# Kernel tuning notes

Measured on AMD Instinct MI355X. Metric: run time of the kernel, lower is better.

The kernel has to match this reference:

```python
import jax, jax.numpy as jnp
import numpy as np

DT = 0.001
TAU_M = 0.02
TAU_S = 0.005
ALPHA = 1.0 - DT / TAU_S  # synaptic decay = 0.8
BETA = 1.0 - DT / TAU_M   # membrane decay = 0.95


def setup_inputs() -> dict:
    key = jax.random.key(0)
    k1, k2 = jax.random.split(key)
    steps, batch, d1, d2 = 100, 256, 784, 512
    x = (jax.random.uniform(k1, (steps, batch, d1)) < 0.05).astype(jnp.float32)
    # kaiming_normal_ on (d2, d1): std = sqrt(2 / fan_in)
    weight = jax.random.normal(k2, (d2, d1), dtype=jnp.float32) * np.float32(np.sqrt(2.0 / d1))
    return {"x": x, "weight": weight}


def reference(x, weight):
    # x: [steps, batch, d1] spikes; weight: [d2, d1]
    batch = x.shape[1]
    d2 = weight.shape[0]
    zeros = jnp.zeros((batch, d2), dtype=x.dtype)

    def step(carry, x_t):
        I_prev, V_prev = carry
        I = ALPHA * I_prev + x_t @ weight.T            # synaptic current
        V_pre = BETA * V_prev + (1.0 - BETA) * I        # membrane before reset
        s = (V_pre > 1.0).astype(x.dtype)               # threshold crossing
        V = (1.0 - s) * V_pre                           # reset to zero on spike
        return (I, V), s

    # torch loop runs i = 1..steps-1 using input[i-1]; output[0] stays zero
    _, spikes = jax.lax.scan(step, (zeros, zeros), x[:-1])
    return jnp.concatenate([zeros[None], spikes], axis=0)  # [steps, batch, d2]
```

## Files before the change

kernel.cpp:

```cpp
#include <hip/hip_runtime.h>

#define STEPS 100
#define BATCH 256
#define D1 784
#define D1P 785
#define D2 512
#define NSTEP 99
#define NTB (NSTEP * BATCH)
#define LIST_PAD 80
#define ROWB 48

#define L1_LISTS_OFF 0
#define L1_LISTS_BYTES ((size_t)NTB * LIST_PAD * 2)
#define L1_CNTS_OFF  L1_LISTS_BYTES
#define L1_CNTS_BYTES ((size_t)NTB * 4)
#define L1_Z_OFF     (((L1_CNTS_OFF + L1_CNTS_BYTES) + 255) & ~(size_t)255)
#define Z_BYTES      ((size_t)NTB * D2 * 4)
#define WS_T1        (L1_Z_OFF + Z_BYTES)

#define WT_BYTES  (D1P * D2 * 4)
#define T2_Z_OFF  ((size_t)((WT_BYTES + 255) & ~255))
#define WS_T2     (T2_Z_OFF + Z_BYTES)

#define HALF1 392
#define HCAP  64


__global__ __launch_bounds__(256) void prep_lists(
    const float* __restrict__ x, unsigned short* __restrict__ lists,
    unsigned int* __restrict__ cnt8s)
{
    const int wid  = blockIdx.x * 4 + (threadIdx.x >> 6);
    const int lane = threadIdx.x & 63;
    const float* xt = x + (size_t)wid * D1;
    unsigned short* lp = lists + (size_t)wid * LIST_PAD;

    int cnt = 0;
    for (int base = 0; base < D1; base += 64) {
        int i = base + lane;
        bool a = (i < D1) && (xt[i] > 0.5f);
        unsigned long long m = __ballot(a);
        int pre = __popcll(m & ((1ull << lane) - 1ull));
        if (a) {
            int p = cnt + pre;
            if (p < LIST_PAD) lp[p] = (unsigned short)(i * ROWB);
        }
        cnt += __popcll(m);
    }
    if (cnt > LIST_PAD) cnt = LIST_PAD;
    int cnt8 = (cnt + 7) & ~7;
    if (cnt8 < 8) cnt8 = 8;
    if (lane < cnt8 - cnt) lp[cnt + lane] = (unsigned short)(D1 * ROWB);
    if (lane == 0) cnt8s[wid] = (unsigned int)cnt8;
}

__global__ __launch_bounds__(512, 8) void gather_lds(
    const float* __restrict__ W,
    const unsigned short* __restrict__ lists,
    const unsigned int* __restrict__ cnt8s,
    float* __restrict__ z)
{
    const int slice = blockIdx.x & 63;
    const int chunk = blockIdx.x >> 6;
    const int j0 = slice * 8;

    __shared__ __align__(16) float wt[D1P * (ROWB / 4)];

    for (int v = threadIdx.x; v < 8 * D1; v += 512) {
        int jj = v & 7;
        int i  = v >> 3;
        wt[i * (ROWB / 4) + jj] = W[(size_t)(j0 + jj) * D1 + i];
    }
    if (threadIdx.x < (ROWB / 4)) wt[D1 * (ROWB / 4) + threadIdx.x] = 0.f;
    __syncthreads();

    const int tbsub = threadIdx.x >> 1;
    const unsigned int jb = (unsigned int)((threadIdx.x & 1) << 4);
    const char* base = (const char*)wt;
    const int tb0 = chunk * (NTB / 16);
    const int tb1 = tb0 + (NTB / 16);

    for (int tb = tb0 + tbsub; tb < tb1; tb += 256) {
        const unsigned short* lp = lists + (size_t)tb * LIST_PAD;
        const int c8 = (int)cnt8s[tb];
        uint4 r = *(const uint4*)lp;
        float ax = 0.f, ay = 0.f, az = 0.f, aw = 0.f;
        float bx = 0.f, by = 0.f, bz = 0.f, bw = 0.f;
        for (int k = 0; k < c8; k += 8) {
            int kn = k + 8;
            if (kn > c8 - 8) kn = c8 - 8;
            uint4 rn = *(const uint4*)(lp + kn);
            float4 w0 = *(const float4*)(base + ((r.x & 0xFFFFu) + jb));
            float4 w1 = *(const float4*)(base + ((r.x >> 16)     + jb));
            float4 w2 = *(const float4*)(base + ((r.y & 0xFFFFu) + jb));
            float4 w3 = *(const float4*)(base + ((r.y >> 16)     + jb));
            float4 w4 = *(const float4*)(base + ((r.z & 0xFFFFu) + jb));
            float4 w5 = *(const float4*)(base + ((r.z >> 16)     + jb));
            float4 w6 = *(const float4*)(base + ((r.w & 0xFFFFu) + jb));
            float4 w7 = *(const float4*)(base + ((r.w >> 16)     + jb));
            ax += w0.x; ay += w0.y; az += w0.z; aw += w0.w;
            bx += w1.x; by += w1.y; bz += w1.z; bw += w1.w;
            ax += w2.x; ay += w2.y; az += w2.z; aw += w2.w;
            bx += w3.x; by += w3.y; bz += w3.z; bw += w3.w;
            ax += w4.x; ay += w4.y; az += w4.z; aw += w4.w;
            bx += w5.x; by += w5.y; bz += w5.z; bw += w5.w;
            ax += w6.x; ay += w6.y; az += w6.z; aw += w6.w;
            bx += w7.x; by += w7.y; bz += w7.z; bw += w7.w;
            r = rn;
        }
        float4 r4;
        r4.x = ax + bx; r4.y = ay + by; r4.z = az + bz; r4.w = aw + bw;
        *(float4*)(z + (size_t)tb * D2 + j0 + ((threadIdx.x & 1) << 2)) = r4;
    }
}

__global__ __launch_bounds__(256) void lif_scan(
    const float* __restrict__ z, float* __restrict__ out)
{
    const int gid = blockIdx.x * 256 + threadIdx.x;
    out[gid] = 0.f;
    float I = 0.f, V = 0.f;
    const float* zp = z + gid;
    float* op = out + (size_t)(BATCH * D2) + gid;
    for (int t0 = 0; t0 < NSTEP; t0 += 8) {
        const int n = (NSTEP - t0 < 8) ? (NSTEP - t0) : 8;
        float zz[8];
        #pragma unroll
        for (int u = 0; u < 8; ++u)
            if (u < n) zz[u] = zp[(size_t)(t0 + u) * (BATCH * D2)];
        #pragma unroll
        for (int u = 0; u < 8; ++u)
            if (u < n) {
                I = 0.8f * I + zz[u];
                float Vp = 0.95f * V + 0.05f * I;
                float s = (Vp > 1.0f) ? 1.0f : 0.f;
                V = (1.0f - s) * Vp;
                op[(size_t)(t0 + u) * (BATCH * D2)] = s;
            }
    }
}

__global__ void transpose_w(const float* __restrict__ W, float* __restrict__ Wt) {
    __shared__ float tile[32][33];
    int i0 = blockIdx.x * 32;
    int j0 = blockIdx.y * 32;
    int tx = threadIdx.x, ty = threadIdx.y;
    for (int r = 0; r < 32; r += 8) {
        int jj = j0 + ty + r, ii = i0 + tx;
        float v = 0.f;
        if (jj < D2 && ii < D1) v = W[jj * D1 + ii];
        tile[ty + r][tx] = v;
    }
    __syncthreads();
    for (int r = 0; r < 32; r += 8) {
        int ii = i0 + ty + r, jj = j0 + tx;
        if (ii < D1P && jj < D2) Wt[ii * D2 + jj] = tile[tx][ty + r];
    }
}

__global__ __launch_bounds__(512) void gather_z(
    const float* __restrict__ x, const float* __restrict__ Wt,
    float* __restrict__ z)
{
    const int g    = threadIdx.x >> 7;
    const int t128 = threadIdx.x & 127;
    const int half = (threadIdx.x >> 6) & 1;
    const int lane = threadIdx.x & 63;
    const int tb   = blockIdx.x * 4 + g;
    __shared__ __align__(16) unsigned int s_off[4][2][HCAP];
    __shared__ int s_cnt[4][2];
    {
        const float* xh = x + (size_t)tb * D1 + half * HALF1;
        unsigned int* lp = s_off[g][half];
        int cnt = 0;
        for (int base = 0; base < HALF1; base += 64) {
            int i = base + lane;
            bool a = (i < HALF1) && (xh[i] > 0.5f);
            unsigned long long m = __ballot(a);
            int pre = __popcll(m & ((1ull << lane) - 1ull));
            if (a) {
                int p = cnt + pre;
                if (p < HCAP) lp[p] = (unsigned int)((half * HALF1 + i) << 11);
            }
            cnt += __popcll(m);
        }
        if (cnt > HCAP) cnt = HCAP;
        int cnt4 = (cnt + 3) & ~3;
        if (lane < cnt4 - cnt) lp[cnt + lane] = (unsigned int)(D1 << 11);
        if (lane == 0) s_cnt[g][half] = cnt4;
    }
    __syncthreads();
    const char* wj = (const char*)Wt + (t128 << 4);
    float ax0 = 0.f, ay0 = 0.f, az0 = 0.f, aw0 = 0.f;
    float ax1 = 0.f, ay1 = 0.f, az1 = 0.f, aw1 = 0.f;
    #pragma unroll
    for (int h = 0; h < 2; ++h) {
        const unsigned int* l = s_off[g][h];
        const int c4 = s_cnt[g][h];
        for (int k = 0; k < c4; k += 4) {
            uint4 o = *(const uint4*)(l + k);
            float4 w0 = *(const float4*)(wj + o.x);
            float4 w1 = *(const float4*)(wj + o.y);
            float4 w2 = *(const float4*)(wj + o.z);
            float4 w3 = *(const float4*)(wj + o.w);
            ax0 += w0.x; ay0 += w0.y; az0 += w0.z; aw0 += w0.w;
            ax1 += w1.x; ay1 += w1.y; az1 += w1.z; aw1 += w1.w;
            ax0 += w2.x; ay0 += w2.y; az0 += w2.z; aw0 += w2.w;
            ax1 += w3.x; ay1 += w3.y; az1 += w3.z; aw1 += w3.w;
        }
    }
    float4 r;
    r.x = ax0 + ax1; r.y = ay0 + ay1; r.z = az0 + az1; r.w = aw0 + aw1;
    *(float4*)(z + (size_t)tb * D2 + (t128 << 2)) = r;
}

__global__ __launch_bounds__(256) void snn_fallback(
    const float* __restrict__ x, const float* __restrict__ Wfull,
    float* __restrict__ out)
{
    const int b = blockIdx.x >> 1;
    const int jhalf = blockIdx.x & 1;
    const int j = jhalf * 256 + threadIdx.x;
    const int lane = threadIdx.x & 63;
    __shared__ int s_cnt;
    __shared__ int s_list[D1];
    out[(size_t)b * D2 + j] = 0.f;
    float I = 0.f, V = 0.f;
    const float* wrow = Wfull + (size_t)j * D1;
    for (int t = 0; t < STEPS - 1; ++t) {
        if (threadIdx.x == 0) s_cnt = 0;
        __syncthreads();
        const float* xt = x + (size_t)(t * BATCH + b) * D1;
        for (int base = 0; base < D1; base += 256) {
            int i = base + threadIdx.x;
            bool active = (i < D1) && (xt[i] > 0.5f);
            unsigned long long mask = __ballot(active);
            int nact = __popcll(mask);
            int pre = __popcll(mask & ((1ull << lane) - 1ull));
            int wb = 0;
            if (lane == 0 && nact) wb = atomicAdd(&s_cnt, nact);
            wb = __shfl(wb, 0);
            if (active) s_list[wb + pre] = i;
        }
        __syncthreads();
        const int cnt = s_cnt;
        float a0 = 0.f, a1 = 0.f, a2 = 0.f, a3 = 0.f;
        int k = 0;
        for (; k + 4 <= cnt; k += 4) {
            a0 += wrow[s_list[k]];     a1 += wrow[s_list[k + 1]];
            a2 += wrow[s_list[k + 2]]; a3 += wrow[s_list[k + 3]];
        }
        for (; k < cnt; ++k) a0 += wrow[s_list[k]];
        float acc = (a0 + a1) + (a2 + a3);
        I = 0.8f * I + acc;
        float Vp = 0.95f * V + 0.05f * I;
        float s = (Vp > 1.0f) ? 1.0f : 0.f;
        V = (1.0f - s) * Vp;
        out[(size_t)(t + 1) * (BATCH * D2) + (size_t)b * D2 + j] = s;
        __syncthreads();
    }
}

extern "C" void kernel_launch(void* const* d_in, const int* in_sizes, int n_in,
                              void* d_out, int out_size, void* d_ws, size_t ws_size,
                              hipStream_t stream) {
    const float* x = (const float*)d_in[0];
    const float* w = (const float*)d_in[1];
    float* out = (float*)d_out;
    char* ws = (char*)d_ws;

    if (ws_size >= WS_T1) {
        unsigned short* lists = (unsigned short*)(ws + L1_LISTS_OFF);
        unsigned int* cnt8s = (unsigned int*)(ws + L1_CNTS_OFF);
        float* z = (float*)(ws + L1_Z_OFF);
        prep_lists<<<NTB / 4, 256, 0, stream>>>(x, lists, cnt8s);
        gather_lds<<<1024, 512, 0, stream>>>(w, lists, cnt8s, z);
        lif_scan<<<BATCH * D2 / 256, 256, 0, stream>>>(z, out);
    } else if (ws_size >= WS_T2) {
        float* wt = (float*)ws;
        float* z  = (float*)(ws + T2_Z_OFF);
        dim3 tg(25, 16), tb(32, 8);
        transpose_w<<<tg, tb, 0, stream>>>(w, wt);
        gather_z<<<NTB / 4, 512, 0, stream>>>(x, wt, z);
        lif_scan<<<BATCH * D2 / 256, 256, 0, stream>>>(z, out);
    } else {
        snn_fallback<<<BATCH * 2, 256, 0, stream>>>(x, w, out);
    }
}
```

Baseline: 224.3 us.

## Widen gather column slice to 32 outputs per block with eight lanes per row

Each gather block now stages a 32-column slice of the transposed weight in about 100 KB of dynamic LDS instead of an 8-column slice. Eight lanes share each (t,b) spike list and each reads a float4 from one LDS row, so list reads and index decoding are spread over 32 outputs rather than 8. Fewer blocks (256) are launched, and the LIF scan is unrolled 16 steps instead of 8 to keep more loads in flight. In exchange, the large LDS footprint limits occupancy to about one block per CU, and 256 blocks may underfill the GPU.

```diff
diff --git a/kernel.cpp b/kernel.cpp
--- a/kernel.cpp
+++ b/kernel.cpp
@@ -8,7 +8,12 @@
 #define NSTEP 99
 #define NTB (NSTEP * BATCH)
 #define LIST_PAD 80
-#define ROWB 48
+
+#define JS 32
+#define ROWB 128
+#define G32_LDS (D1P * JS * 4)
+#define NCHUNK 16
+#define CHUNK_TB (NTB / NCHUNK)
 
 #define L1_LISTS_OFF 0
 #define L1_LISTS_BYTES ((size_t)NTB * LIST_PAD * 2)
@@ -43,44 +48,56 @@
         int pre = __popcll(m & ((1ull << lane) - 1ull));
         if (a) {
             int p = cnt + pre;
-            if (p < LIST_PAD) lp[p] = (unsigned short)(i * ROWB);
+            if (p < LIST_PAD) lp[p] = (unsigned short)(i << 3);
         }
         cnt += __popcll(m);
     }
     if (cnt > LIST_PAD) cnt = LIST_PAD;
     int cnt8 = (cnt + 7) & ~7;
     if (cnt8 < 8) cnt8 = 8;
-    if (lane < cnt8 - cnt) lp[cnt + lane] = (unsigned short)(D1 * ROWB);
+    if (lane < cnt8 - cnt) lp[cnt + lane] = (unsigned short)(D1 << 3);
     if (lane == 0) cnt8s[wid] = (unsigned int)cnt8;
 }
 
-__global__ __launch_bounds__(512, 8) void gather_lds(
+__global__ __launch_bounds__(512) void gather32(
     const float* __restrict__ W,
     const unsigned short* __restrict__ lists,
     const unsigned int* __restrict__ cnt8s,
     float* __restrict__ z)
 {
-    const int slice = blockIdx.x & 63;
-    const int chunk = blockIdx.x >> 6;
-    const int j0 = slice * 8;
-
-    __shared__ __align__(16) float wt[D1P * (ROWB / 4)];
-
-    for (int v = threadIdx.x; v < 8 * D1; v += 512) {
-        int jj = v & 7;
-        int i  = v >> 3;
-        wt[i * (ROWB / 4) + jj] = W[(size_t)(j0 + jj) * D1 + i];
-    }
-    if (threadIdx.x < (ROWB / 4)) wt[D1 * (ROWB / 4) + threadIdx.x] = 0.f;
+    const int slice = blockIdx.x & 15;
+    const int chunk = blockIdx.x >> 4;
+    const int j0 = slice * JS;
+
+    extern __shared__ float wt[];
+
+    {
+        const int jj = threadIdx.x & 31;
+        const int ih = threadIdx.x >> 5;
+        const float* wrow = W + (size_t)(j0 + jj) * D1;
+        for (int it = 0; it < 13; ++it) {
+            int i4 = ih + it * 16;
+            if (i4 < 196) {
+                int i = i4 * 4;
+                float4 v = *(const float4*)(wrow + i);
+                wt[(i + 0) * JS + jj] = v.x;
+                wt[(i + 1) * JS + jj] = v.y;
+                wt[(i + 2) * JS + jj] = v.z;
+                wt[(i + 3) * JS + jj] = v.w;
+            }
+        }
+        if (threadIdx.x < JS) wt[D1 * JS + threadIdx.x] = 0.f;
+    }
     __syncthreads();
 
-    const int tbsub = threadIdx.x >> 1;
-    const unsigned int jb = (unsigned int)((threadIdx.x & 1) << 4);
+    const int lane = threadIdx.x & 63;
+    const int wv   = threadIdx.x >> 6;
+    const int grp  = lane >> 3;
+    const unsigned qd16 = (unsigned)((lane & 7) << 4);
     const char* base = (const char*)wt;
-    const int tb0 = chunk * (NTB / 16);
-    const int tb1 = tb0 + (NTB / 16);
-
-    for (int tb = tb0 + tbsub; tb < tb1; tb += 256) {
+
+    const int tb_end = (chunk + 1) * CHUNK_TB;
+    for (int tb = chunk * CHUNK_TB + wv * 8 + grp; tb < tb_end; tb += 64) {
         const unsigned short* lp = lists + (size_t)tb * LIST_PAD;
         const int c8 = (int)cnt8s[tb];
         uint4 r = *(const uint4*)lp;
@@ -90,14 +107,14 @@
             int kn = k + 8;
             if (kn > c8 - 8) kn = c8 - 8;
             uint4 rn = *(const uint4*)(lp + kn);
-            float4 w0 = *(const float4*)(base + ((r.x & 0xFFFFu) + jb));
-            float4 w1 = *(const float4*)(base + ((r.x >> 16)     + jb));
-            float4 w2 = *(const float4*)(base + ((r.y & 0xFFFFu) + jb));
-            float4 w3 = *(const float4*)(base + ((r.y >> 16)     + jb));
-            float4 w4 = *(const float4*)(base + ((r.z & 0xFFFFu) + jb));
-            float4 w5 = *(const float4*)(base + ((r.z >> 16)     + jb));
-            float4 w6 = *(const float4*)(base + ((r.w & 0xFFFFu) + jb));
-            float4 w7 = *(const float4*)(base + ((r.w >> 16)     + jb));
+            float4 w0 = *(const float4*)(base + (((r.x & 0xFFFFu) << 4) + qd16));
+            float4 w1 = *(const float4*)(base + (((r.x >> 16)     << 4) + qd16));
+            float4 w2 = *(const float4*)(base + (((r.y & 0xFFFFu) << 4) + qd16));
+            float4 w3 = *(const float4*)(base + (((r.y >> 16)     << 4) + qd16));
+            float4 w4 = *(const float4*)(base + (((r.z & 0xFFFFu) << 4) + qd16));
+            float4 w5 = *(const float4*)(base + (((r.z >> 16)     << 4) + qd16));
+            float4 w6 = *(const float4*)(base + (((r.w & 0xFFFFu) << 4) + qd16));
+            float4 w7 = *(const float4*)(base + (((r.w >> 16)     << 4) + qd16));
             ax += w0.x; ay += w0.y; az += w0.z; aw += w0.w;
             bx += w1.x; by += w1.y; bz += w1.z; bw += w1.w;
             ax += w2.x; ay += w2.y; az += w2.z; aw += w2.w;
@@ -110,7 +127,7 @@
         }
         float4 r4;
         r4.x = ax + bx; r4.y = ay + by; r4.z = az + bz; r4.w = aw + bw;
-        *(float4*)(z + (size_t)tb * D2 + j0 + ((threadIdx.x & 1) << 2)) = r4;
+        *(float4*)(z + (size_t)tb * D2 + j0 + (int)(qd16 >> 2)) = r4;
     }
 }
 
@@ -122,14 +139,14 @@
     float I = 0.f, V = 0.f;
     const float* zp = z + gid;
     float* op = out + (size_t)(BATCH * D2) + gid;
-    for (int t0 = 0; t0 < NSTEP; t0 += 8) {
-        const int n = (NSTEP - t0 < 8) ? (NSTEP - t0) : 8;
-        float zz[8];
+    for (int t0 = 0; t0 < NSTEP; t0 += 16) {
+        const int n = (NSTEP - t0 < 16) ? (NSTEP - t0) : 16;
+        float zz[16];
         #pragma unroll
-        for (int u = 0; u < 8; ++u)
+        for (int u = 0; u < 16; ++u)
             if (u < n) zz[u] = zp[(size_t)(t0 + u) * (BATCH * D2)];
         #pragma unroll
-        for (int u = 0; u < 8; ++u)
+        for (int u = 0; u < 16; ++u)
             if (u < n) {
                 I = 0.8f * I + zz[u];
                 float Vp = 0.95f * V + 0.05f * I;
@@ -270,11 +287,17 @@
     char* ws = (char*)d_ws;
 
     if (ws_size >= WS_T1) {
+        static bool g32_init = false;
+        if (!g32_init) {
+            (void)hipFuncSetAttribute((const void*)gather32,
+                hipFuncAttributeMaxDynamicSharedMemorySize, G32_LDS);
+            g32_init = true;
+        }
         unsigned short* lists = (unsigned short*)(ws + L1_LISTS_OFF);
         unsigned int* cnt8s = (unsigned int*)(ws + L1_CNTS_OFF);
         float* z = (float*)(ws + L1_Z_OFF);
         prep_lists<<<NTB / 4, 256, 0, stream>>>(x, lists, cnt8s);
-        gather_lds<<<1024, 512, 0, stream>>>(w, lists, cnt8s, z);
+        gather32<<<256, 512, G32_LDS, stream>>>(w, lists, cnt8s, z);
         lif_scan<<<BATCH * D2 / 256, 256, 0, stream>>>(z, out);
     } else if (ws_size >= WS_T2) {
         float* wt = (float*)ws;
```

Result: slower. 230.4 us (+2.7%).
